# Optimization experiments

Hardware: AMD Instinct MI355X
Metric: run time of the kernel (lower is better)

## Reference

```python
import jax, jax.numpy as jnp
import numpy as np

B, DM, NH, NL, NP = 4, 768, 12, 3, 4
HD = DM // NH
H_IMG, W_IMG = 896, 896
LEVELS = [(H_IMG // 8, W_IMG // 8), (H_IMG // 16, W_IMG // 16), (H_IMG // 32, W_IMG // 32)]
QH, QW = H_IMG // 14, W_IMG // 14
LQ = QH * QW            # 4096 query tokens (stride-14 ViT grid)
LIN = sum(h * w for h, w in LEVELS)  # 16464 multi-scale value tokens


def setup_inputs() -> dict:
    key = jax.random.key(0)
    ks = jax.random.split(key, 14)
    s = 0.02
    return {
        "query": jax.random.normal(ks[0], (B, LQ, DM), jnp.float32),
        "feat": jax.random.normal(ks[1], (B, LIN, DM), jnp.float32),
        "ln_q_g": jnp.ones((DM,), jnp.float32),
        "ln_q_b": jnp.zeros((DM,), jnp.float32),
        "ln_f_g": jnp.ones((DM,), jnp.float32),
        "ln_f_b": jnp.zeros((DM,), jnp.float32),
        "W_off": jax.random.normal(ks[2], (DM, NH * NL * NP * 2), jnp.float32) * s,
        "b_off": jax.random.normal(ks[3], (NH * NL * NP * 2,), jnp.float32) * s,
        "W_attn": jax.random.normal(ks[4], (DM, NH * NL * NP), jnp.float32) * s,
        "b_attn": jax.random.normal(ks[5], (NH * NL * NP,), jnp.float32) * s,
        "W_val": jax.random.normal(ks[6], (DM, DM), jnp.float32) * s,
        "b_val": jnp.zeros((DM,), jnp.float32),
        "W_out": jax.random.normal(ks[7], (DM, DM), jnp.float32) * s,
        "b_out": jnp.zeros((DM,), jnp.float32),
        "gamma": jax.random.normal(ks[8], (DM,), jnp.float32) * s,
    }


def _ln(x, g, b, eps=1e-6):
    m = x.mean(-1, keepdims=True)
    v = ((x - m) ** 2).mean(-1, keepdims=True)
    return (x - m) * jax.lax.rsqrt(v + eps) * g + b


def _ref_points():
    # get_reference_points for the stride-14 query grid; pixel-center coords normalized
    ry, rx = jnp.meshgrid(
        (jnp.arange(QH, dtype=jnp.float32) + 0.5) / QH,
        (jnp.arange(QW, dtype=jnp.float32) + 0.5) / QW,
        indexing="ij",
    )
    return jnp.stack([rx.reshape(-1), ry.reshape(-1)], -1)  # (LQ, 2) in (x, y)


def _sample_level(v, loc, h_, w_):
    # v: (B, h_, w_, NH, HD); loc: (B, LQ, NH, NP, 2) normalized [0,1]
    # torch grid_sample bilinear, align_corners=False, zero padding
    x = loc[..., 0] * w_ - 0.5
    y = loc[..., 1] * h_ - 0.5
    x0 = jnp.floor(x)
    y0 = jnp.floor(y)
    wx = (x - x0)[..., None]
    wy = (y - y0)[..., None]
    x0i = x0.astype(jnp.int32)
    y0i = y0.astype(jnp.int32)
    bi = jnp.arange(B)[:, None, None, None]
    hi = jnp.arange(NH)[None, None, :, None]

    def g(yi, xi):
        valid = ((xi >= 0) & (xi < w_) & (yi >= 0) & (yi < h_)).astype(v.dtype)
        got = v[bi, jnp.clip(yi, 0, h_ - 1), jnp.clip(xi, 0, w_ - 1), hi]  # (B,LQ,NH,NP,HD)
        return got * valid[..., None]

    v00 = g(y0i, x0i)
    v01 = g(y0i, x0i + 1)
    v10 = g(y0i + 1, x0i)
    v11 = g(y0i + 1, x0i + 1)
    return v00 * (1 - wx) * (1 - wy) + v01 * wx * (1 - wy) + v10 * (1 - wx) * wy + v11 * wx * wy


def _injector(query, feat, ln_q_g, ln_q_b, ln_f_g, ln_f_b, W_off, b_off, W_attn, b_attn,
              W_val, b_val, W_out, b_out, gamma):
    q = _ln(query, ln_q_g, ln_q_b)
    f = _ln(feat, ln_f_g, ln_f_b)
    value = (f @ W_val + b_val).reshape(B, LIN, NH, HD)
    off = (q @ W_off + b_off).reshape(B, LQ, NH, NL, NP, 2)
    aw = jax.nn.softmax((q @ W_attn + b_attn).reshape(B, LQ, NH, NL * NP), axis=-1)
    aw = aw.reshape(B, LQ, NH, NL, NP)
    ref = _ref_points()  # (LQ, 2)
    offset_norm = jnp.array([[w, h] for h, w in LEVELS], jnp.float32)  # (NL, 2) = (W_, H_)
    loc = ref[None, :, None, None, None, :] + off / offset_norm[None, None, None, :, None, :]
    outs = []
    start = 0
    for lvl, (h_, w_) in enumerate(LEVELS):
        v = value[:, start:start + h_ * w_].reshape(B, h_, w_, NH, HD)
        outs.append(_sample_level(v, loc[:, :, :, lvl], h_, w_))
        start += h_ * w_
    samp = jnp.stack(outs, axis=3)  # (B, LQ, NH, NL, NP, HD)
    attn_out = (samp * aw[..., None]).sum(axis=(3, 4)).reshape(B, LQ, DM)
    attn_out = attn_out @ W_out + b_out
    return query + gamma * attn_out


def reference(query, feat, ln_q_g, ln_q_b, ln_f_g, ln_f_b, W_off, b_off, W_attn, b_attn,
              W_val, b_val, W_out, b_out, gamma):
    return _injector(query, feat, ln_q_g, ln_q_b, ln_f_g, ln_f_b, W_off, b_off, W_attn,
                     b_attn, W_val, b_val, W_out, b_out, gamma)
```

## Files before the change

kernel.cpp:

```cpp
#include <hip/hip_runtime.h>
#include <hip/hip_bf16.h>

typedef __hip_bfloat16 bf16;

#define BB    4
#define LQ    4096
#define LIN   16464
#define DM    768
#define NH    12
#define HD    64
#define K_DIM 768

typedef __attribute__((ext_vector_type(8))) __bf16 bfrag;
typedef __attribute__((ext_vector_type(4))) float  ffrag;

__device__ __forceinline__ void g2l16(const void* g, void* l) {
    __builtin_amdgcn_global_load_lds(
        (const __attribute__((address_space(1))) void*)g,
        (__attribute__((address_space(3))) void*)l, 16, 0, 0);
}

__device__ __forceinline__ int xcd_swz(int orig, int nwg) {
    int xcd = orig & 7, within = orig >> 3;
    int q = nwg >> 3, r = nwg & 7;
    return (xcd < r ? xcd * (q + 1) : r * (q + 1) + (xcd - r) * q) + within;
}

__global__ __launch_bounds__(256) void ln_kernel(
    const float* __restrict__ x, const float* __restrict__ g,
    const float* __restrict__ beta, bf16* __restrict__ y)
{
    int r = blockIdx.x * 4 + (threadIdx.x >> 6);
    int lane = threadIdx.x & 63;
    const float4* xr = (const float4*)(x + (size_t)r * DM);
    float4 v[3];
    #pragma unroll
    for (int i = 0; i < 3; i++) v[i] = xr[lane + 64 * i];
    float s = 0.f, ss = 0.f;
    #pragma unroll
    for (int i = 0; i < 3; i++) {
        s  += v[i].x + v[i].y + v[i].z + v[i].w;
        ss += v[i].x * v[i].x + v[i].y * v[i].y + v[i].z * v[i].z + v[i].w * v[i].w;
    }
    #pragma unroll
    for (int m = 1; m <= 32; m <<= 1) {
        s  += __shfl_xor(s, m);
        ss += __shfl_xor(ss, m);
    }
    float mean = s * (1.f / DM);
    float inv  = rsqrtf(ss * (1.f / DM) - mean * mean + 1e-6f);
    bf16* yr = y + (size_t)r * DM;
    #pragma unroll
    for (int i = 0; i < 3; i++) {
        float4 gg = ((const float4*)g)[lane + 64 * i];
        float4 bb = ((const float4*)beta)[lane + 64 * i];
        union { bf16 h[4]; uint2 u; } p;
        p.h[0] = __float2bfloat16((v[i].x - mean) * inv * gg.x + bb.x);
        p.h[1] = __float2bfloat16((v[i].y - mean) * inv * gg.y + bb.y);
        p.h[2] = __float2bfloat16((v[i].z - mean) * inv * gg.z + bb.z);
        p.h[3] = __float2bfloat16((v[i].w - mean) * inv * gg.w + bb.w);
        *(uint2*)(yr + (lane + 64 * i) * 4) = p.u;
    }
}

__global__ __launch_bounds__(256) void cast_transpose(
    const float* __restrict__ W, bf16* __restrict__ Wt, int N)
{
    __shared__ float t[32][33];
    int n0 = blockIdx.x * 32, k0 = blockIdx.y * 32;
    int tx = threadIdx.x & 31, ty = threadIdx.x >> 5;
    #pragma unroll
    for (int i = 0; i < 4; i++) {
        int k = k0 + ty + i * 8;
        int n = n0 + tx;
        t[ty + i * 8][tx] = (n < N) ? W[(size_t)k * N + n] : 0.f;
    }
    __syncthreads();
    #pragma unroll
    for (int i = 0; i < 4; i++) {
        int n = n0 + ty + i * 8;
        Wt[(size_t)n * K_DIM + k0 + tx] = __float2bfloat16(t[tx][ty + i * 8]);
    }
}

__global__ __launch_bounds__(512) void gemm256_value(
    const bf16*  __restrict__ A,
    const bf16*  __restrict__ Bt,
    const float* __restrict__ bias,
    bf16*        __restrict__ C,
    int M, int N)
{
    __shared__ __align__(16) char lds[131072];

    int tid  = threadIdx.x;
    int lane = tid & 63;
    int wave = tid >> 6;

    int nwg  = gridDim.x * gridDim.y;
    int orig = blockIdx.y * gridDim.x + blockIdx.x;
    int wg   = xcd_swz(orig, nwg);
    int bn = (wg % gridDim.x) * 256;
    int bm = (wg / gridDim.x) * 256;

    int ahalf = wave >> 2;
    int wc    = (wave & 3) * 64;
    int bhalf = (wave & 3) >> 1;
    int bcb   = (wave & 1) * 64;

    int ln15 = lane & 15, g = lane >> 4, l7 = lane & 7;

    ffrag acc[8][4] = {};

    int r_loc = tid >> 3;
    int koff  = (((tid & 7) ^ (r_loc & 7)) * 8);

    const bf16* gA[2][2];
    const bf16* gB[2][2];
    #pragma unroll
    for (int h = 0; h < 2; h++)
        #pragma unroll
        for (int ld = 0; ld < 2; ld++) {
            int ra = min(bm + h * 128 + ld * 64 + r_loc, M - 1);
            gA[h][ld] = A  + (size_t)ra * K_DIM + koff;
            int cb = bn + h * 128 + ld * 64 + r_loc;
            gB[h][ld] = Bt + (size_t)cb * K_DIM + koff;
        }

    auto stageA = [&](char* buf, int h, int kt) {
        g2l16(gA[h][0] + kt * 64, buf + h * 16384 + tid * 16);
        g2l16(gA[h][1] + kt * 64, buf + h * 16384 + 8192 + tid * 16);
    };
    auto stageB = [&](char* buf, int h, int kt) {
        g2l16(gB[h][0] + kt * 64, buf + 32768 + h * 16384 + tid * 16);
        g2l16(gB[h][1] + kt * 64, buf + 32768 + h * 16384 + 8192 + tid * 16);
    };

    stageA(lds, 0, 0); stageA(lds, 1, 0); stageB(lds, 0, 0); stageB(lds, 1, 0);

    int sby[2];
    sby[0] = ((0 * 4 + g) ^ l7) * 16;
    sby[1] = ((1 * 4 + g) ^ l7) * 16;

    #pragma unroll
    for (int kt = 0; kt < 12; kt++) {
        char* cur = lds + (kt & 1) * 65536;
        char* nxt = lds + ((kt & 1) ^ 1) * 65536;
        const char* Ac = cur + ahalf * 16384;
        const char* Bc = cur + 32768 + bhalf * 16384;

        if (kt + 1 < 12) {
            stageA(nxt, 0, kt + 1);
            asm volatile("s_waitcnt vmcnt(2)" ::: "memory");
        } else {
            asm volatile("s_waitcnt vmcnt(0)" ::: "memory");
        }
        __builtin_amdgcn_s_barrier();

        bfrag bf[4][2];
        #pragma unroll
        for (int nc = 0; nc < 4; nc++)
            #pragma unroll
            for (int ks = 0; ks < 2; ks++)
                bf[nc][ks] = *(const bfrag*)(Bc + (bcb + nc * 16 + ln15) * 128 + sby[ks]);
        {
            bfrag af[2][2];
            #pragma unroll
            for (int m2 = 0; m2 < 2; m2++)
                #pragma unroll
                for (int ks = 0; ks < 2; ks++)
                    af[m2][ks] = *(const bfrag*)(Ac + (m2 * 16 + ln15) * 128 + sby[ks]);
            __builtin_amdgcn_s_setprio(1);
            #pragma unroll
            for (int m2 = 0; m2 < 2; m2++)
                #pragma unroll
                for (int nc = 0; nc < 4; nc++)
                    #pragma unroll
                    for (int ks = 0; ks < 2; ks++)
                        acc[m2][nc] = __builtin_amdgcn_mfma_f32_16x16x32_bf16(
                            af[m2][ks], bf[nc][ks], acc[m2][nc], 0, 0, 0);
            __builtin_amdgcn_s_setprio(0);
        }
        __builtin_amdgcn_s_barrier();

        #pragma unroll
        for (int qd = 1; qd < 4; qd++) {
            if (kt + 1 < 12) {
                if (qd == 1) stageA(nxt, 1, kt + 1);
                else if (qd == 2) stageB(nxt, 0, kt + 1);
                else stageB(nxt, 1, kt + 1);
            }
            bfrag af[2][2];
            #pragma unroll
            for (int m2 = 0; m2 < 2; m2++)
                #pragma unroll
                for (int ks = 0; ks < 2; ks++)
                    af[m2][ks] = *(const bfrag*)(Ac + ((qd * 2 + m2) * 16 + ln15) * 128 + sby[ks]);
            __builtin_amdgcn_s_setprio(1);
            #pragma unroll
            for (int m2 = 0; m2 < 2; m2++)
                #pragma unroll
                for (int nc = 0; nc < 4; nc++)
                    #pragma unroll
                    for (int ks = 0; ks < 2; ks++)
                        acc[qd * 2 + m2][nc] = __builtin_amdgcn_mfma_f32_16x16x32_bf16(
                            af[m2][ks], bf[nc][ks], acc[qd * 2 + m2][nc], 0, 0, 0);
            __builtin_amdgcn_s_setprio(0);
            __builtin_amdgcn_s_barrier();
        }
    }

    int q4 = g * 4;
    #pragma unroll
    for (int mr = 0; mr < 8; mr++) {
        #pragma unroll
        for (int rr = 0; rr < 4; rr++) {
            int rg = bm + ahalf * 128 + mr * 16 + q4 + rr;
            if (rg < M) {
                #pragma unroll
                for (int nc = 0; nc < 4; nc++) {
                    int cg = bn + wc + nc * 16 + ln15;
                    C[(size_t)rg * N + cg] =
                        __float2bfloat16(acc[mr][nc][rr] + bias[cg]);
                }
            }
        }
    }
}

__device__ __forceinline__ void gemm128_body(
    const bf16*  __restrict__ A,
    const bf16*  __restrict__ Bt,
    const float* __restrict__ bias,
    void*        __restrict__ C,
    const float* __restrict__ resid,
    const float* __restrict__ gamma,
    const float* __restrict__ bias2,
    int M, int N, int mode, int nsplit, char* lds)
{
    int tid  = threadIdx.x;
    int lane = tid & 63;

    int nwg  = gridDim.x * gridDim.y;
    int orig = blockIdx.y * gridDim.x + blockIdx.x;
    int wg = xcd_swz(orig, nwg);
    int bn = (wg % gridDim.x) * 128;
    int bm = (wg / gridDim.x) * 128;

    int wave = tid >> 6;
    int wr = (wave & 1) * 64, wc = (wave >> 1) * 64;

    ffrag acc[4][4] = {};

    int rA = tid >> 2;
    int kb = (((tid & 3) ^ ((rA >> 1) & 3)) * 8);
    int ra0 = min(bm + rA, M - 1), ra1 = min(bm + 64 + rA, M - 1);
    const bf16* gA0 = A  + (size_t)ra0 * K_DIM + kb;
    const bf16* gA1 = A  + (size_t)ra1 * K_DIM + kb;
    const bf16* gB0 = Bt + (size_t)(bn + rA) * K_DIM + kb;
    const bf16* gB1 = Bt + (size_t)(bn + 64 + rA) * K_DIM + kb;

    int mrow = lane & 15;
    int kqs  = (((lane >> 4) ^ ((mrow >> 1) & 3)) * 8);

    auto stage = [&](char* buf, int kt) {
        const int ko = kt * 32;
        g2l16(gA0 + ko, buf + tid * 16);
        g2l16(gA1 + ko, buf + tid * 16 + 4096);
        g2l16(gB0 + ko, buf + 8192 + tid * 16);
        g2l16(gB1 + ko, buf + 8192 + tid * 16 + 4096);
    };

    stage(lds, 0);
    asm volatile("s_waitcnt vmcnt(0)" ::: "memory");
    __builtin_amdgcn_s_barrier();

    #pragma unroll
    for (int kt = 0; kt < 24; kt++) {
        char* cur = lds + (kt & 1) * 16384;
        char* nxt = lds + ((kt & 1) ^ 1) * 16384;
        if (kt + 1 < 24) stage(nxt, kt + 1);

        bfrag a[4], b[4];
        #pragma unroll
        for (int t = 0; t < 4; t++) {
            a[t] = *(const bfrag*)(cur + ((wr + t * 16 + mrow) * 32 + kqs) * 2);
            b[t] = *(const bfrag*)(cur + 8192 + ((wc + t * 16 + mrow) * 32 + kqs) * 2);
        }
        __builtin_amdgcn_s_setprio(1);
        #pragma unroll
        for (int i = 0; i < 4; i++)
            #pragma unroll
            for (int j = 0; j < 4; j++)
                acc[i][j] = __builtin_amdgcn_mfma_f32_16x16x32_bf16(
                    a[i], b[j], acc[i][j], 0, 0, 0);
        __builtin_amdgcn_s_setprio(0);

        asm volatile("s_waitcnt vmcnt(0)" ::: "memory");
        __builtin_amdgcn_s_barrier();
    }

    int q4 = (lane >> 4) * 4;
    #pragma unroll
    for (int i = 0; i < 4; i++) {
        #pragma unroll
        for (int rr = 0; rr < 4; rr++) {
            int rg = bm + wr + i * 16 + q4 + rr;
            if (rg < M) {
                #pragma unroll
                for (int j = 0; j < 4; j++) {
                    int cg = bn + wc + j * 16 + mrow;
                    if (cg < N) {
                        float bv = (mode == 3 && cg >= nsplit) ? bias2[cg - nsplit]
                                                               : bias[cg];
                        float v = acc[i][j][rr] + bv;
                        size_t idx = (size_t)rg * N + cg;
                        if (mode == 2)      ((float*)C)[idx] = resid[idx] + gamma[cg] * v;
                        else                ((float*)C)[idx] = v;
                    }
                }
            }
        }
    }
}

__global__ __launch_bounds__(256) void gemm128_comb(
    const bf16* __restrict__ A, const bf16* __restrict__ Bt,
    const float* __restrict__ bias, void* __restrict__ C,
    const float* __restrict__ bias2, int M, int N, int nsplit)
{
    __shared__ __align__(16) char lds[32768];
    gemm128_body(A, Bt, bias, C, nullptr, nullptr, bias2, M, N, 3, nsplit, lds);
}

__global__ __launch_bounds__(256) void gemm128_out(
    const bf16* __restrict__ A, const bf16* __restrict__ Bt,
    const float* __restrict__ bias, void* __restrict__ C,
    const float* __restrict__ resid, const float* __restrict__ gamma,
    int M, int N)
{
    __shared__ __align__(16) char lds[32768];
    gemm128_body(A, Bt, bias, C, resid, gamma, nullptr, M, N, 2, 0, lds);
}

__global__ __launch_bounds__(256) void prep_kernel(
    const float* __restrict__ comb, uint4* __restrict__ pre)
{
    int t  = blockIdx.x * 256 + threadIdx.x;
    int p  = t % 12;
    int uh = t / 12;
    int h  = uh % NH;
    int bq = uh / NH;
    int q  = bq & (LQ - 1);
    int b  = bq >> 12;

    const float* rowp = comb + (size_t)bq * 432;
    const float* lg = rowp + 288 + h * 12;

    float4 a4 = ((const float4*)lg)[0];
    float4 b4 = ((const float4*)lg)[1];
    float4 c4 = ((const float4*)lg)[2];
    float mx = fmaxf(fmaxf(fmaxf(fmaxf(a4.x, a4.y), fmaxf(a4.z, a4.w)),
                           fmaxf(fmaxf(b4.x, b4.y), fmaxf(b4.z, b4.w))),
                     fmaxf(fmaxf(c4.x, c4.y), fmaxf(c4.z, c4.w)));
    float den = __expf(a4.x - mx) + __expf(a4.y - mx) + __expf(a4.z - mx) +
                __expf(a4.w - mx) + __expf(b4.x - mx) + __expf(b4.y - mx) +
                __expf(b4.z - mx) + __expf(b4.w - mx) + __expf(c4.x - mx) +
                __expf(c4.y - mx) + __expf(c4.z - mx) + __expf(c4.w - mx);
    float lp  = lg[p];
    float awn = __expf(lp - mx) / den;

    int lvl = p >> 2;
    const int wl = (lvl == 0) ? 112 : (lvl == 1 ? 56 : 28);
    const int sl = (lvl == 0) ? 0   : (lvl == 1 ? 12544 : 15680);

    float2 oxy = *(const float2*)(rowp + h * 24 + p * 2);

    float rx = ((q & 63) + 0.5f) * (1.f / 64.f);
    float ry = ((q >> 6) + 0.5f) * (1.f / 64.f);
    float x = rx * wl + oxy.x - 0.5f;
    float y = ry * wl + oxy.y - 0.5f;
    float xf = floorf(x), yf = floorf(y);
    float wx = x - xf, wy = y - yf;
    int x0 = (int)xf, x1 = x0 + 1;
    int y0 = (int)yf, y1 = y0 + 1;
    bool vx0 = (unsigned)x0 < (unsigned)wl, vx1 = (unsigned)x1 < (unsigned)wl;
    bool vy0 = (unsigned)y0 < (unsigned)wl, vy1 = (unsigned)y1 < (unsigned)wl;
    int x0c = min(max(x0, 0), wl - 1), x1c = min(max(x1, 0), wl - 1);
    int y0c = min(max(y0, 0), wl - 1), y1c = min(max(y1, 0), wl - 1);

    int base = b * LIN + sl;
    int yb0 = (base + y0c * wl) * (NH * HD) + h * HD;
    int yb1 = (base + y1c * wl) * (NH * HD) + h * HD;
    int xb0 = x0c * (NH * HD);
    int xb1 = x1c * (NH * HD);

    float w0x = vx0 ? (1.f - wx) * awn : 0.f;
    float w1x = vx1 ? wx * awn : 0.f;
    float wy0f = vy0 ? (1.f - wy) : 0.f;
    float wy1f = vy1 ? wy : 0.f;

    uint4 i4 = {(unsigned)yb0, (unsigned)yb1, (unsigned)xb0, (unsigned)xb1};
    uint4 w4 = {__float_as_uint(w0x), __float_as_uint(w1x),
                __float_as_uint(wy0f), __float_as_uint(wy1f)};
    pre[(size_t)t * 2 + 0] = i4;
    pre[(size_t)t * 2 + 1] = w4;
}

__global__ __launch_bounds__(256) void sample_kernel(
    const bf16*  __restrict__ value,
    const uint4* __restrict__ pre,
    bf16*        __restrict__ attn)
{
    __shared__ float red[4][8][64];

    int wv   = threadIdx.x >> 6;
    int wg   = xcd_swz(blockIdx.x, gridDim.x);
    int unit = __builtin_amdgcn_readfirstlane((wg << 2) + wv);
    int lane = threadIdx.x & 63;
    int o   = lane & 7;
    int c8  = lane >> 3;
    int k   = c8 & 3;
    bool dx = (k & 1) != 0, dy = (k >> 1) != 0;
    bool hi = (c8 & 4) != 0;
    int h  = unit % NH;
    int bq = unit / NH;

    const uint4* pp = pre + (size_t)unit * 24;
    const bf16*  vbase = value + o * 8;

    float acc[8] = {0.f};

    #pragma unroll
    for (int it = 0; it < 6; it++) {
        const uint4* rec = pp + it * 4 + (hi ? 2 : 0);
        uint4 i4 = rec[0];
        uint4 w4 = rec[1];
        int idx = (dy ? (int)i4.y : (int)i4.x) + (dx ? (int)i4.w : (int)i4.z);
        float w = (dx ? __uint_as_float(w4.y) : __uint_as_float(w4.x)) *
                  (dy ? __uint_as_float(w4.w) : __uint_as_float(w4.z));
        uint4 v = *(const uint4*)(vbase + idx);
        const unsigned* u = (const unsigned*)&v;
        #pragma unroll
        for (int j = 0; j < 4; j++) {
            float f0 = __uint_as_float(u[j] << 16);
            float f1 = __uint_as_float(u[j] & 0xFFFF0000u);
            acc[j * 2 + 0] = fmaf(w, f0, acc[j * 2 + 0]);
            acc[j * 2 + 1] = fmaf(w, f1, acc[j * 2 + 1]);
        }
    }

    {
        float* rw = &red[wv][c8][0];
        int base = (o * 8 + c8 * 4) & 63;
        *(float4*)&rw[base] = float4{acc[0], acc[1], acc[2], acc[3]};
        *(float4*)&rw[(base + 4) & 63] = float4{acc[4], acc[5], acc[6], acc[7]};
    }
    asm volatile("s_waitcnt lgkmcnt(0)" ::: "memory");
    __builtin_amdgcn_sched_barrier(0);
    float sum = 0.f;
    #pragma unroll
    for (int s = 0; s < 8; s++)
        sum += red[wv][s][(lane + s * 4) & 63];

    attn[(size_t)bq * DM + h * HD + lane] = __float2bfloat16(sum);
}

extern "C" void kernel_launch(void* const* d_in, const int* in_sizes, int n_in,
                              void* d_out, int out_size, void* d_ws, size_t ws_size,
                              hipStream_t stream)
{
    const float* query  = (const float*)d_in[0];
    const float* feat   = (const float*)d_in[1];
    const float* ln_q_g = (const float*)d_in[2];
    const float* ln_q_b = (const float*)d_in[3];
    const float* ln_f_g = (const float*)d_in[4];
    const float* ln_f_b = (const float*)d_in[5];
    const float* W_off  = (const float*)d_in[6];
    const float* b_off  = (const float*)d_in[7];
    const float* W_attn = (const float*)d_in[8];
    const float* b_attn = (const float*)d_in[9];
    const float* W_val  = (const float*)d_in[10];
    const float* b_val  = (const float*)d_in[11];
    const float* W_out  = (const float*)d_in[12];
    const float* b_out  = (const float*)d_in[13];
    const float* gamma  = (const float*)d_in[14];
    float* out = (float*)d_out;

    char* ws = (char*)d_ws;
    char* od = (char*)d_out;
    const int M_F = BB * LIN;
    const int M_Q = BB * LQ;

    bf16*  value  = (bf16*)(ws);
    bf16*  f_ln   = (bf16*)(ws + 101154816);
    bf16*  Wt_out = (bf16*)(ws + 101154816);
    uint4* pre    = (uint4*)(ws + 101154816 + 4194304);
    bf16*  q_ln   = (bf16*)(ws + 202309632);
    bf16*  attn   = (bf16*)(ws + 202309632);

    bf16*  Wt_val  = (bf16*)(od);
    bf16*  Wt_comb = (bf16*)(od + 1179648);
    float* comb    = (float*)(od + 2162688);

    cast_transpose<<<dim3(24, 24), 256, 0, stream>>>(W_val, Wt_val, 768);
    cast_transpose<<<dim3(9, 24), 256, 0, stream>>>(W_off, Wt_comb, 288);
    cast_transpose<<<dim3(7, 24), 256, 0, stream>>>(
        W_attn, Wt_comb + (size_t)288 * K_DIM, 144);

    ln_kernel<<<M_F / 4, 256, 0, stream>>>(feat, ln_f_g, ln_f_b, f_ln);
    ln_kernel<<<M_Q / 4, 256, 0, stream>>>(query, ln_q_g, ln_q_b, q_ln);

    gemm256_value<<<dim3(3, (M_F + 255) / 256), 512, 0, stream>>>(
        f_ln, Wt_val, b_val, value, M_F, DM);

    cast_transpose<<<dim3(24, 24), 256, 0, stream>>>(W_out, Wt_out, 768);

    gemm128_comb<<<dim3(4, M_Q / 128), 256, 0, stream>>>(
        q_ln, Wt_comb, b_off, comb, b_attn, M_Q, 432, 288);

    prep_kernel<<<(M_Q * NH * 12) / 256, 256, 0, stream>>>(comb, pre);

    sample_kernel<<<(M_Q * NH) / 4, 256, 0, stream>>>(value, pre, attn);

    gemm128_out<<<dim3(6, M_Q / 128), 256, 0, stream>>>(
        attn, Wt_out, b_out, out, query, gamma, M_Q, DM);
}
```

Baseline: 696.5 us.

## Restructure value GEMM into triple-buffered K=32 pipeline with simpler swizzle

Rewrites the 256x256 value-projection GEMM main loop. It now uses three LDS stages of K=32 each (96KB) in place of two K=64 stages with quarter-phased staging, and waits on vmcnt so that two tiles stay in flight. Each K step loads all A/B fragments once and issues 32 MFMAs. The aim is deeper prefetch with fewer barriers per FLOP, at the cost of more loop iterations and barriers per K and a new XOR swizzle that may cause LDS bank conflicts.

```diff
diff --git a/kernel.cpp b/kernel.cpp
--- a/kernel.cpp
+++ b/kernel.cpp
@@ -90,7 +90,7 @@
     bf16*        __restrict__ C,
     int M, int N)
 {
-    __shared__ __align__(16) char lds[131072];
+    __shared__ __align__(16) char lds[98304];
 
     int tid  = threadIdx.x;
     int lane = tid & 63;
@@ -104,112 +104,65 @@
 
     int ahalf = wave >> 2;
     int wc    = (wave & 3) * 64;
-    int bhalf = (wave & 3) >> 1;
-    int bcb   = (wave & 1) * 64;
-
-    int ln15 = lane & 15, g = lane >> 4, l7 = lane & 7;
+
+    int mrow = lane & 15;
+    int kqs  = (((lane >> 4) ^ ((mrow >> 1) & 3)) * 8);
 
     ffrag acc[8][4] = {};
 
-    int r_loc = tid >> 3;
-    int koff  = (((tid & 7) ^ (r_loc & 7)) * 8);
-
-    const bf16* gA[2][2];
-    const bf16* gB[2][2];
-    #pragma unroll
-    for (int h = 0; h < 2; h++)
-        #pragma unroll
-        for (int ld = 0; ld < 2; ld++) {
-            int ra = min(bm + h * 128 + ld * 64 + r_loc, M - 1);
-            gA[h][ld] = A  + (size_t)ra * K_DIM + koff;
-            int cb = bn + h * 128 + ld * 64 + r_loc;
-            gB[h][ld] = Bt + (size_t)cb * K_DIM + koff;
-        }
-
-    auto stageA = [&](char* buf, int h, int kt) {
-        g2l16(gA[h][0] + kt * 64, buf + h * 16384 + tid * 16);
-        g2l16(gA[h][1] + kt * 64, buf + h * 16384 + 8192 + tid * 16);
+    int rA = tid >> 2;
+    int kb = (((tid & 3) ^ ((rA >> 1) & 3)) * 8);
+    int ra0 = min(bm + rA, M - 1), ra1 = min(bm + 128 + rA, M - 1);
+    const bf16* gA0 = A  + (size_t)ra0 * K_DIM + kb;
+    const bf16* gA1 = A  + (size_t)ra1 * K_DIM + kb;
+    const bf16* gB0 = Bt + (size_t)(bn + rA) * K_DIM + kb;
+    const bf16* gB1 = Bt + (size_t)(bn + 128 + rA) * K_DIM + kb;
+
+    auto stage = [&](char* buf, int kt) {
+        const int ko = kt * 32;
+        g2l16(gA0 + ko, buf + tid * 16);
+        g2l16(gA1 + ko, buf + tid * 16 + 8192);
+        g2l16(gB0 + ko, buf + 16384 + tid * 16);
+        g2l16(gB1 + ko, buf + 16384 + tid * 16 + 8192);
     };
-    auto stageB = [&](char* buf, int h, int kt) {
-        g2l16(gB[h][0] + kt * 64, buf + 32768 + h * 16384 + tid * 16);
-        g2l16(gB[h][1] + kt * 64, buf + 32768 + h * 16384 + 8192 + tid * 16);
-    };
-
-    stageA(lds, 0, 0); stageA(lds, 1, 0); stageB(lds, 0, 0); stageB(lds, 1, 0);
-
-    int sby[2];
-    sby[0] = ((0 * 4 + g) ^ l7) * 16;
-    sby[1] = ((1 * 4 + g) ^ l7) * 16;
-
-    #pragma unroll
-    for (int kt = 0; kt < 12; kt++) {
-        char* cur = lds + (kt & 1) * 65536;
-        char* nxt = lds + ((kt & 1) ^ 1) * 65536;
-        const char* Ac = cur + ahalf * 16384;
-        const char* Bc = cur + 32768 + bhalf * 16384;
-
-        if (kt + 1 < 12) {
-            stageA(nxt, 0, kt + 1);
-            asm volatile("s_waitcnt vmcnt(2)" ::: "memory");
-        } else {
-            asm volatile("s_waitcnt vmcnt(0)" ::: "memory");
-        }
+
+    char* b0 = lds;
+    char* b1 = lds + 32768;
+    char* b2 = lds + 65536;
+    stage(b0, 0); stage(b1, 1); stage(b2, 2);
+
+    #pragma unroll
+    for (int kt = 0; kt < 24; kt++) {
+        if (kt + 2 < 24)      asm volatile("s_waitcnt vmcnt(8)" ::: "memory");
+        else if (kt + 1 < 24) asm volatile("s_waitcnt vmcnt(4)" ::: "memory");
+        else                  asm volatile("s_waitcnt vmcnt(0)" ::: "memory");
         __builtin_amdgcn_s_barrier();
 
-        bfrag bf[4][2];
+        const char* Ab = b0 + (ahalf * 128) * 64;
+        const char* Bb = b0 + 16384 + wc * 64;
+        bfrag af[8], bf[4];
+        #pragma unroll
+        for (int mr = 0; mr < 8; mr++)
+            af[mr] = *(const bfrag*)(Ab + (mr * 16 + mrow) * 64 + kqs * 2);
         #pragma unroll
         for (int nc = 0; nc < 4; nc++)
+            bf[nc] = *(const bfrag*)(Bb + (nc * 16 + mrow) * 64 + kqs * 2);
+
+        __builtin_amdgcn_s_setprio(1);
+        #pragma unroll
+        for (int mr = 0; mr < 8; mr++)
             #pragma unroll
-            for (int ks = 0; ks < 2; ks++)
-                bf[nc][ks] = *(const bfrag*)(Bc + (bcb + nc * 16 + ln15) * 128 + sby[ks]);
-        {
-            bfrag af[2][2];
-            #pragma unroll
-            for (int m2 = 0; m2 < 2; m2++)
-                #pragma unroll
-                for (int ks = 0; ks < 2; ks++)
-                    af[m2][ks] = *(const bfrag*)(Ac + (m2 * 16 + ln15) * 128 + sby[ks]);
-            __builtin_amdgcn_s_setprio(1);
-            #pragma unroll
-            for (int m2 = 0; m2 < 2; m2++)
-                #pragma unroll
-                for (int nc = 0; nc < 4; nc++)
-                    #pragma unroll
-                    for (int ks = 0; ks < 2; ks++)
-                        acc[m2][nc] = __builtin_amdgcn_mfma_f32_16x16x32_bf16(
-                            af[m2][ks], bf[nc][ks], acc[m2][nc], 0, 0, 0);
-            __builtin_amdgcn_s_setprio(0);
-        }
+            for (int nc = 0; nc < 4; nc++)
+                acc[mr][nc] = __builtin_amdgcn_mfma_f32_16x16x32_bf16(
+                    af[mr], bf[nc], acc[mr][nc], 0, 0, 0);
+        __builtin_amdgcn_s_setprio(0);
+
         __builtin_amdgcn_s_barrier();
-
-        #pragma unroll
-        for (int qd = 1; qd < 4; qd++) {
-            if (kt + 1 < 12) {
-                if (qd == 1) stageA(nxt, 1, kt + 1);
-                else if (qd == 2) stageB(nxt, 0, kt + 1);
-                else stageB(nxt, 1, kt + 1);
-            }
-            bfrag af[2][2];
-            #pragma unroll
-            for (int m2 = 0; m2 < 2; m2++)
-                #pragma unroll
-                for (int ks = 0; ks < 2; ks++)
-                    af[m2][ks] = *(const bfrag*)(Ac + ((qd * 2 + m2) * 16 + ln15) * 128 + sby[ks]);
-            __builtin_amdgcn_s_setprio(1);
-            #pragma unroll
-            for (int m2 = 0; m2 < 2; m2++)
-                #pragma unroll
-                for (int nc = 0; nc < 4; nc++)
-                    #pragma unroll
-                    for (int ks = 0; ks < 2; ks++)
-                        acc[qd * 2 + m2][nc] = __builtin_amdgcn_mfma_f32_16x16x32_bf16(
-                            af[m2][ks], bf[nc][ks], acc[qd * 2 + m2][nc], 0, 0, 0);
-            __builtin_amdgcn_s_setprio(0);
-            __builtin_amdgcn_s_barrier();
-        }
-    }
-
-    int q4 = g * 4;
+        if (kt + 3 < 24) stage(b0, kt + 3);
+        char* tp = b0; b0 = b1; b1 = b2; b2 = tp;
+    }
+
+    int q4 = (lane >> 4) * 4;
     #pragma unroll
     for (int mr = 0; mr < 8; mr++) {
         #pragma unroll
@@ -218,7 +171,7 @@
             if (rg < M) {
                 #pragma unroll
                 for (int nc = 0; nc < 4; nc++) {
-                    int cg = bn + wc + nc * 16 + ln15;
+                    int cg = bn + wc + nc * 16 + mrow;
                     C[(size_t)rg * N + cg] =
                         __float2bfloat16(acc[mr][nc][rr] + bias[cg]);
                 }
```

Measured after the change: 708.4 us. About the same (+1.7%).
